# Kernel optimization log

Measured on AMD Instinct MI355X. Metric: run time of the kernel, lower is better.

The kernel has to match this reference:

```python
import jax, jax.numpy as jnp
import numpy as np

B, C, N = 8, 512, 2048
C4 = C // 4


def setup_inputs() -> dict:
    key = jax.random.key(0)
    ks = jax.random.split(key, 10)
    s = lambda fan: 1.0 / np.sqrt(fan)
    return {
        "x": jax.random.normal(ks[0], (B, C, N), jnp.float32),
        "query": jax.random.normal(ks[1], (B, C, N), jnp.float32),
        "mask": jax.random.randint(ks[2], (B, N), 0, 2, jnp.int32),
        "wqk": jax.random.normal(ks[3], (C4, C), jnp.float32) * s(C),  # shared q/k 1x1 conv
        "wv": jax.random.normal(ks[4], (C, C), jnp.float32) * s(C),
        "bv": jax.random.normal(ks[5], (C,), jnp.float32) * 0.01,
        "wt": jax.random.normal(ks[6], (C, C), jnp.float32) * s(C),
        "bt": jax.random.normal(ks[7], (C,), jnp.float32) * 0.01,
        "gamma": jnp.ones((C,), jnp.float32),
        "beta": jnp.zeros((C,), jnp.float32),
        "rmean": jax.random.normal(ks[8], (C,), jnp.float32) * 0.01,
        "rvar": jax.random.uniform(ks[9], (C,), jnp.float32, 0.5, 1.5),
    }


def reference(x, query, mask, wqk, wv, bv, wt, bt, gamma, beta, rmean, rvar):
    # 1x1 convs == per-point linears (q and k share weights)
    x_q = jnp.einsum("dc,bcn->bnd", wqk, query)            # [B,N,C4]
    x_k = jnp.einsum("dc,bcn->bdn", wqk, x)                # [B,C4,N]
    x_v = jnp.einsum("dc,bcn->bdn", wv, x) + bv[None, :, None]  # [B,C,N]

    energy = jnp.einsum("bnd,bdm->bnm", x_q, x_k)          # [B,N,N]
    m = mask.astype(bool)
    m2 = m[:, :, None] & m[:, None, :]                     # [B,N,N]
    energy = jnp.where(m2, energy, jnp.float32(-9e15))
    d = 1e-9 + m2.sum(axis=1, keepdims=True).astype(energy.dtype)  # [B,1,N]
    attention = jax.nn.softmax(energy / d, axis=-1)

    x_r = jnp.einsum("bcn,bnm->bcm", x_v, attention)       # [B,C,N]
    h = x - x_r
    h = jnp.einsum("dc,bcn->bdn", wt, h) + bt[None, :, None]
    # BatchNorm1d (eval) + ReLU
    inv = gamma / jnp.sqrt(rvar + 1e-5)
    h = (h - rmean[None, :, None]) * inv[None, :, None] + beta[None, :, None]
    h = jax.nn.relu(h)
    return x + h
```

## Files before the change

### kernel.cpp

```cpp
#include <hip/hip_runtime.h>
#include <math.h>

typedef __bf16 bf16;
typedef bf16 bf16x8 __attribute__((ext_vector_type(8)));
typedef bf16 bf16x4 __attribute__((ext_vector_type(4)));
typedef float f32x4 __attribute__((ext_vector_type(4)));
typedef unsigned long long u64;

constexpr int kB = 8, kC = 512, kC4 = 128, kN = 2048;

#define MFMA16(a, b, c) __builtin_amdgcn_mfma_f32_16x16x32_bf16(a, b, c, 0, 0, 0)
#define MFMA8(a, b, c) \
  __builtin_amdgcn_mfma_f32_16x16x32_fp8_fp8(a, b, c, 0, 0, 0)

__device__ __forceinline__ unsigned pack4_fp8(float a, float b, float c,
                                              float d) {
  unsigned v = 0;
  v = __builtin_amdgcn_cvt_pk_fp8_f32(a, b, v, false);
  v = __builtin_amdgcn_cvt_pk_fp8_f32(c, d, v, true);
  return v;
}

__global__ __launch_bounds__(256) void k_prep(
    const int* __restrict__ mask, const float* __restrict__ wqk,
    const float* __restrict__ wv, const float* __restrict__ wt,
    const float* __restrict__ gamma, const float* __restrict__ rvar,
    float* __restrict__ cnt, bf16* __restrict__ wqk_bf,
    bf16* __restrict__ wv_bf, bf16* __restrict__ wt_bf,
    float* __restrict__ invg, float* __restrict__ Ssum) {
  const int t = threadIdx.x;
  if (blockIdx.x < 8) {
    const int b = blockIdx.x;
    int s = 0;
    for (int i = t; i < kN; i += 256) s += mask[b * kN + i];
    __shared__ int red[256];
    red[t] = s;
    __syncthreads();
    for (int off = 128; off > 0; off >>= 1) {
      if (t < off) red[t] += red[t + off];
      __syncthreads();
    }
    if (t == 0) cnt[b] = (float)red[0];
    return;
  }
  const int total = 65536 + 262144 + 262144 + 512 + 16384;
  for (int i = (blockIdx.x - 8) * 256 + t; i < total; i += 128 * 256) {
    if (i < 65536) {
      wqk_bf[i] = (bf16)wqk[i];
    } else if (i < 327680) {
      wv_bf[i - 65536] = (bf16)wv[i - 65536];
    } else if (i < 589824) {
      wt_bf[i - 327680] = (bf16)wt[i - 327680];
    } else if (i < 590336) {
      const int j = i - 589824;
      invg[j] = gamma[j] * rsqrtf(rvar[j] + 1e-5f);
    } else {
      Ssum[i - 590336] = 0.0f;
    }
  }
}

__global__ __launch_bounds__(256) void k_tr2(const float* __restrict__ Q,
                                             const float* __restrict__ X,
                                             bf16* __restrict__ XTq,
                                             bf16* __restrict__ XTx) {
  __shared__ float tile[32][69];
  const int z = blockIdx.z, b = z & 7;
  const float* Xs = (z < 8) ? Q : X;
  bf16* XT = (z < 8) ? XTq : XTx;
  const int c0 = blockIdx.y * 32, n0 = blockIdx.x * 64;
  const int t = threadIdx.x;
  const int cc = t >> 4, n4 = (t & 15) * 4;
#pragma unroll
  for (int p = 0; p < 2; p++) {
    const int c = p * 16 + cc;
    const f32x4 v =
        *(const f32x4*)&Xs[((size_t)(b * kC + c0 + c)) * kN + n0 + n4];
    tile[c][n4 + 0] = v[0];
    tile[c][n4 + 1] = v[1];
    tile[c][n4 + 2] = v[2];
    tile[c][n4 + 3] = v[3];
  }
  __syncthreads();
  const int n = t >> 2, c8 = (t & 3) * 8;
  bf16x8 o;
#pragma unroll
  for (int j = 0; j < 8; j++) o[j] = (bf16)tile[c8 + j][n];
  *(bf16x8*)&XT[((size_t)(b * kN + n0 + n)) * kC + c0 + c8] = o;
}

__global__ __launch_bounds__(256, 2) void k_projQK(
    const bf16* __restrict__ XTq, const bf16* __restrict__ XTx,
    const bf16* __restrict__ W, bf16* __restrict__ qT, bf16* __restrict__ kT) {
  __shared__ __align__(16) bf16 As[2][128][32];
  __shared__ __align__(16) bf16 Bs[2][128][32];
  const int nb = blockIdx.x, b = blockIdx.y, src = blockIdx.z;
  const bf16* XT = src ? XTx : XTq;
  bf16* OT = src ? kT : qT;
  const int n0 = nb * 128;
  const int t_ = threadIdx.x, w = t_ >> 6, l = t_ & 63, lo4 = l & 15, g = l >> 4;
  const int mh = w >> 1, ch = w & 1;
  const int srow = w * 16 + (l >> 2), sch = l & 3;
  const int spos = sch ^ ((l >> 3) & 3);
  const int rpos = g ^ ((lo4 >> 1) & 3);
  const bf16* gA0 = &XT[((size_t)(b * kN + n0 + srow)) * kC + sch * 8];
  const bf16* gA1 = gA0 + (size_t)64 * kC;
  const bf16* gB0 = &W[(size_t)srow * kC + sch * 8];
  const bf16* gB1 = gB0 + (size_t)64 * kC;
  f32x4 acc[4][4] = {};
  bf16x8 ra0, ra1, rb0, rb1;
  ra0 = *(const bf16x8*)&gA0[0];
  ra1 = *(const bf16x8*)&gA1[0];
  rb0 = *(const bf16x8*)&gB0[0];
  rb1 = *(const bf16x8*)&gB1[0];
  *(bf16x8*)&As[0][srow][spos * 8] = ra0;
  *(bf16x8*)&As[0][srow + 64][spos * 8] = ra1;
  *(bf16x8*)&Bs[0][srow][spos * 8] = rb0;
  *(bf16x8*)&Bs[0][srow + 64][spos * 8] = rb1;
  __syncthreads();
  for (int tt = 0; tt < 16; tt++) {
    const int buf = tt & 1;
    if (tt < 15) {
      const int k0 = (tt + 1) * 32;
      ra0 = *(const bf16x8*)&gA0[k0];
      ra1 = *(const bf16x8*)&gA1[k0];
      rb0 = *(const bf16x8*)&gB0[k0];
      rb1 = *(const bf16x8*)&gB1[k0];
    }
    bf16x8 af[4], bfr[4];
#pragma unroll
    for (int nf = 0; nf < 4; nf++)
      af[nf] = *(const bf16x8*)&As[buf][mh * 64 + nf * 16 + lo4][rpos * 8];
#pragma unroll
    for (int cf = 0; cf < 4; cf++)
      bfr[cf] = *(const bf16x8*)&Bs[buf][ch * 64 + cf * 16 + lo4][rpos * 8];
#pragma unroll
    for (int nf = 0; nf < 4; nf++)
#pragma unroll
      for (int cf = 0; cf < 4; cf++)
        acc[nf][cf] = MFMA16(af[nf], bfr[cf], acc[nf][cf]);
    if (tt < 15) {
      *(bf16x8*)&As[buf ^ 1][srow][spos * 8] = ra0;
      *(bf16x8*)&As[buf ^ 1][srow + 64][spos * 8] = ra1;
      *(bf16x8*)&Bs[buf ^ 1][srow][spos * 8] = rb0;
      *(bf16x8*)&Bs[buf ^ 1][srow + 64][spos * 8] = rb1;
    }
    __syncthreads();
  }
  bf16* bncw = ((bf16*)As) + w * 16 * 72;
#pragma unroll
  for (int nf = 0; nf < 4; nf++) {
    const int nbase = n0 + mh * 64 + nf * 16;
#pragma unroll
    for (int cf = 0; cf < 4; cf++)
#pragma unroll
      for (int r = 0; r < 4; r++)
        bncw[(4 * g + r) * 72 + cf * 16 + lo4] = (bf16)acc[nf][cf][r];
    const int rr = l >> 2, seg = (l & 3) * 16;
    const bf16x8 v0 = *(const bf16x8*)&bncw[rr * 72 + seg];
    const bf16x8 v1 = *(const bf16x8*)&bncw[rr * 72 + seg + 8];
    bf16* orow = &OT[((size_t)(b * kN + nbase + rr)) * kC4 + ch * 64 + seg];
    *(bf16x8*)&orow[0] = v0;
    *(bf16x8*)&orow[8] = v1;
  }
}

__global__ __launch_bounds__(256, 2) void k_projV(
    const bf16* __restrict__ XTx, const bf16* __restrict__ Wv,
    const float* __restrict__ bv, bf16* __restrict__ xv2) {
  __shared__ __align__(16) bf16 As[2][128][32];
  __shared__ __align__(16) bf16 Bs[2][128][32];
  const int blk = blockIdx.x;
  const int b = blk & 7, tile = blk >> 3;
  const int cb = tile & 3, nb = tile >> 2;
  const int n0 = nb * 128, c0 = cb * 128;
  const int t_ = threadIdx.x, w = t_ >> 6, l = t_ & 63, lo4 = l & 15, g = l >> 4;
  const int mh = w >> 1, ch = w & 1;
  const int srow = w * 16 + (l >> 2), sch = l & 3;
  const int spos = sch ^ ((l >> 3) & 3);
  const int rpos = g ^ ((lo4 >> 1) & 3);
  const bf16* gA0 = &XTx[((size_t)(b * kN + n0 + srow)) * kC + sch * 8];
  const bf16* gA1 = gA0 + (size_t)64 * kC;
  const bf16* gB0 = &Wv[(size_t)(c0 + srow) * kC + sch * 8];
  const bf16* gB1 = gB0 + (size_t)64 * kC;
  f32x4 acc[4][4] = {};
  bf16x8 ra0, ra1, rb0, rb1;
  ra0 = *(const bf16x8*)&gA0[0];
  ra1 = *(const bf16x8*)&gA1[0];
  rb0 = *(const bf16x8*)&gB0[0];
  rb1 = *(const bf16x8*)&gB1[0];
  *(bf16x8*)&As[0][srow][spos * 8] = ra0;
  *(bf16x8*)&As[0][srow + 64][spos * 8] = ra1;
  *(bf16x8*)&Bs[0][srow][spos * 8] = rb0;
  *(bf16x8*)&Bs[0][srow + 64][spos * 8] = rb1;
  __syncthreads();
  for (int tt = 0; tt < 16; tt++) {
    const int buf = tt & 1;
    if (tt < 15) {
      const int k0 = (tt + 1) * 32;
      ra0 = *(const bf16x8*)&gA0[k0];
      ra1 = *(const bf16x8*)&gA1[k0];
      rb0 = *(const bf16x8*)&gB0[k0];
      rb1 = *(const bf16x8*)&gB1[k0];
    }
    bf16x8 af[4], bfr[4];
#pragma unroll
    for (int nf = 0; nf < 4; nf++)
      af[nf] = *(const bf16x8*)&As[buf][mh * 64 + nf * 16 + lo4][rpos * 8];
#pragma unroll
    for (int cf = 0; cf < 4; cf++)
      bfr[cf] = *(const bf16x8*)&Bs[buf][ch * 64 + cf * 16 + lo4][rpos * 8];
#pragma unroll
    for (int nf = 0; nf < 4; nf++)
#pragma unroll
      for (int cf = 0; cf < 4; cf++)
        acc[nf][cf] = MFMA16(af[nf], bfr[cf], acc[nf][cf]);
    if (tt < 15) {
      *(bf16x8*)&As[buf ^ 1][srow][spos * 8] = ra0;
      *(bf16x8*)&As[buf ^ 1][srow + 64][spos * 8] = ra1;
      *(bf16x8*)&Bs[buf ^ 1][srow][spos * 8] = rb0;
      *(bf16x8*)&Bs[buf ^ 1][srow + 64][spos * 8] = rb1;
    }
    __syncthreads();
  }
#pragma unroll
  for (int cf = 0; cf < 4; cf++) {
    const int c = c0 + ch * 64 + cf * 16 + lo4;
    const float bvv = bv[c];
#pragma unroll
    for (int nf = 0; nf < 4; nf++) {
      const int nbase = n0 + mh * 64 + nf * 16 + g * 4;
      bf16x4 o;
#pragma unroll
      for (int r = 0; r < 4; r++) o[r] = (bf16)(acc[nf][cf][r] + bvv);
      *(bf16x4*)&xv2[(((size_t)b * 32 + (nbase >> 6)) * kC + c) * 64 +
                     (nbase & 63)] = o;
    }
  }
}

__global__ __launch_bounds__(256) void k_sum(
    const bf16* __restrict__ qT, const bf16* __restrict__ kT,
    const int* __restrict__ mask, const float* __restrict__ cnt,
    unsigned char* __restrict__ UT8, float* __restrict__ Ssum) {
  __shared__ __align__(16) bf16 kts[2][64][128];
  __shared__ __align__(16) unsigned Ubuf[64][16];
  __shared__ int mss[2][64];
  const int blk = blockIdx.x;
  const int b = blk & 7, nb = (blk >> 3) & 31, mh2 = blk >> 8;
  const int m00 = mh2 * 1024;
  const int t_ = threadIdx.x, w = t_ >> 6, l = t_ & 63, lo4 = l & 15, g = l >> 4;
  const float invd = 1.0f / (cnt[b] + 1e-9f);
  const int n0 = nb * 64;
  bf16x8 aq[4];
#pragma unroll
  for (int ks = 0; ks < 4; ks++)
    aq[ks] = *(const bf16x8*)&qT[((size_t)(b * kN + n0 + w * 16 + lo4)) * kC4 +
                                 ks * 32 + g * 8];
  const int nq = n0 + w * 16 + g * 4;
  const int4 mi = *(const int4*)&mask[b * kN + nq];
  const int mn4[4] = {mi.x, mi.y, mi.z, mi.w};
  float rs4[4] = {0.0f, 0.0f, 0.0f, 0.0f};
  bf16x8 rg[4];
#pragma unroll
  for (int i = 0; i < 4; i++) {
    const int row = w * 16 + i * 4 + g;
    const int q = (l & 15) ^ (row & 7);
    rg[i] = *(const bf16x8*)&kT[((size_t)(b * kN + m00 + row)) * kC4 + q * 8];
  }
#pragma unroll
  for (int i = 0; i < 4; i++) {
    const int row = w * 16 + i * 4 + g;
    *(bf16x8*)&kts[0][row][(l & 15) * 8] = rg[i];
  }
  if (t_ < 16)
    *(int4*)&mss[0][t_ * 4] = *(const int4*)&mask[b * kN + m00 + t_ * 4];
  __syncthreads();
  for (int tt = 0; tt < 16; tt++) {
    const int buf = tt & 1;
    if (tt < 15) {
      const int m0 = m00 + (tt + 1) * 64;
#pragma unroll
      for (int i = 0; i < 4; i++) {
        const int row = w * 16 + i * 4 + g;
        const int q = (l & 15) ^ (row & 7);
        rg[i] = *(const bf16x8*)&kT[((size_t)(b * kN + m0 + row)) * kC4 + q * 8];
      }
    }
#pragma unroll
    for (int mf = 0; mf < 4; mf++) {
      f32x4 e = {};
#pragma unroll
      for (int ks = 0; ks < 4; ks++) {
        const bf16x8 bk =
            *(const bf16x8*)&kts[buf][mf * 16 + lo4]
                                 [((ks * 4 + g) ^ (lo4 & 7)) * 8];
        e = MFMA16(aq[ks], bk, e);
      }
      const int mmv = mss[buf][mf * 16 + lo4];
      float u[4];
#pragma unroll
      for (int r = 0; r < 4; r++) {
        u[r] = mmv ? (mn4[r] ? __expf(e[r] * invd) : 1.0f) : 0.0f;
        rs4[r] += u[r];
      }
      Ubuf[mf * 16 + lo4][(w * 4 + g) ^ lo4] =
          pack4_fp8(u[0], u[1], u[2], u[3]);
    }
    __syncthreads();
    if (tt < 15) {
#pragma unroll
      for (int i = 0; i < 4; i++) {
        const int row = w * 16 + i * 4 + g;
        *(bf16x8*)&kts[buf ^ 1][row][(l & 15) * 8] = rg[i];
      }
      if (t_ < 16)
        *(int4*)&mss[buf ^ 1][t_ * 4] =
            *(const int4*)&mask[b * kN + m00 + (tt + 1) * 64 + t_ * 4];
    }
    {
      const int row = t_ >> 2, q = t_ & 3;
      int4 pkt;
      pkt.x = (int)Ubuf[row][(q * 4 + 0) ^ (row & 15)];
      pkt.y = (int)Ubuf[row][(q * 4 + 1) ^ (row & 15)];
      pkt.z = (int)Ubuf[row][(q * 4 + 2) ^ (row & 15)];
      pkt.w = (int)Ubuf[row][(q * 4 + 3) ^ (row & 15)];
      *(int4*)&UT8[((size_t)(b * kN + m00 + tt * 64 + row)) * kN + n0 +
                   q * 16] = pkt;
    }
    __syncthreads();
  }
#pragma unroll
  for (int r = 0; r < 4; r++) {
#pragma unroll
    for (int off = 1; off < 16; off <<= 1) rs4[r] += __shfl_xor(rs4[r], off);
  }
  if (lo4 == 0) {
#pragma unroll
    for (int r = 0; r < 4; r++) atomicAdd(&Ssum[b * kN + nq + r], rs4[r]);
  }
}

__global__ __launch_bounds__(256) void k_scale(const bf16* __restrict__ xv2,
                                               const float* __restrict__ Ssum,
                                               unsigned* __restrict__ xv8) {
  const int blk = blockIdx.x;
  const int b = blk & 7, part = blk >> 3;
  const size_t base = (size_t)b * (32 * kC * 64);
  for (int it = 0; it < 4; it++) {
    const int chunk = part * 1024 + it * 256 + threadIdx.x;
    const size_t e = (size_t)chunk * 8;
    const int n = ((int)(e >> 15)) * 64 + ((int)e & 63);
    const bf16x8 v = *(const bf16x8*)&xv2[base + e];
    const f32x4 ss0 = *(const f32x4*)&Ssum[b * kN + n];
    const f32x4 ss1 = *(const f32x4*)&Ssum[b * kN + n + 4];
    f32x4 s0, s1;
#pragma unroll
    for (int j = 0; j < 4; j++) {
      s0[j] = 1.0f / ss0[j];
      s1[j] = 1.0f / ss1[j];
    }
    uint2 o;
    o.x = pack4_fp8((float)v[0] * s0[0], (float)v[1] * s0[1],
                    (float)v[2] * s0[2], (float)v[3] * s0[3]);
    o.y = pack4_fp8((float)v[4] * s1[0], (float)v[5] * s1[1],
                    (float)v[6] * s1[2], (float)v[7] * s1[3]);
    *(uint2*)&xv8[(base + e) >> 2] = o;
  }
}

__global__ __launch_bounds__(256, 2) void k_attn2(
    const unsigned char* __restrict__ UT8,
    const unsigned char* __restrict__ xv8, const float* __restrict__ x,
    bf16* __restrict__ hT) {
  __shared__ __align__(16) unsigned char As[2][128][128];
  __shared__ __align__(16) unsigned char Bs[2][128][128];
  const int blk = blockIdx.x;
  const int b = blk & 7, tile = blk >> 3;
  const int cb = tile & 3, mb = tile >> 2;
  const int m0 = mb * 128, c0 = cb * 128;
  const int t_ = threadIdx.x, w = t_ >> 6, l = t_ & 63, lo4 = l & 15, g = l >> 4;
  const int mh = w >> 1, ch = w & 1;
  const int srow = t_ >> 1, psl = t_ & 1;
  const int swk = srow & 15;
  const unsigned char* gA = &UT8[((size_t)(b * kN + m0 + srow)) * kN + psl * 64];
  const unsigned char* gB =
      &xv8[(((size_t)b * 32 + psl) * kC + c0 + srow) * 64];
  f32x4 acc[4][4] = {};
  ulonglong2 eA[4], eB[4], oA[4], oB[4];
#define LOADSET(RA, RB, T)                                                     \
  {                                                                            \
    _Pragma("unroll") for (int q = 0; q < 4; q++) {                            \
      RA[q] = *(const ulonglong2*)&gA[(size_t)(T)*128 + q * 16];               \
      RB[q] = *(const ulonglong2*)&gB[(size_t)(T)*65536 + q * 16];             \
    }                                                                          \
  }
#define STORE_TILE(BUF, RA, RB)                                                \
  {                                                                            \
    _Pragma("unroll") for (int j = 0; j < 8; j++) {                            \
      const int v = (psl * 8 + j) ^ swk;                                       \
      const u64 va = (j & 1) ? RA[j >> 1].y : RA[j >> 1].x;                    \
      const u64 vb = (j & 1) ? RB[j >> 1].y : RB[j >> 1].x;                    \
      *(u64*)&As[BUF][srow][v * 8] = va;                                       \
      *(u64*)&Bs[BUF][srow][v * 8] = vb;                                       \
    }                                                                          \
  }
#define FRAGS_MFMA(BUF)                                                        \
  {                                                                            \
    _Pragma("unroll") for (int ks = 0; ks < 4; ks++) {                         \
      long af[4], bfr[4];                                                      \
      _Pragma("unroll") for (int mf = 0; mf < 4; mf++) af[mf] =                \
          *(const long*)&As[BUF][mh * 64 + mf * 16 + lo4]                      \
                            [((ks * 4 + g) ^ lo4) * 8];                        \
      _Pragma("unroll") for (int cf = 0; cf < 4; cf++) bfr[cf] =               \
          *(const long*)&Bs[BUF][ch * 64 + cf * 16 + lo4]                      \
                            [((ks * 4 + g) ^ lo4) * 8];                        \
      _Pragma("unroll") for (int mf = 0; mf < 4; mf++)                         \
          _Pragma("unroll") for (int cf = 0; cf < 4; cf++) acc[mf][cf] =       \
              MFMA8(af[mf], bfr[cf], acc[mf][cf]);                             \
    }                                                                          \
  }
  LOADSET(eA, eB, 0);
  STORE_TILE(0, eA, eB);
  LOADSET(oA, oB, 1);
  __syncthreads();
  for (int tt2 = 0; tt2 < 16; tt2 += 2) {
    if (tt2 + 2 < 16) LOADSET(eA, eB, tt2 + 2);
    FRAGS_MFMA(0);
    STORE_TILE(1, oA, oB);
    __syncthreads();
    if (tt2 + 3 < 16) LOADSET(oA, oB, tt2 + 3);
    FRAGS_MFMA(1);
    if (tt2 + 2 < 16) STORE_TILE(0, eA, eB);
    __syncthreads();
  }
#undef FRAGS_MFMA
#undef STORE_TILE
#undef LOADSET
  bf16* bncw = ((bf16*)As) + w * 16 * 72;
#pragma unroll
  for (int mf = 0; mf < 4; mf++) {
    const int mbase = m0 + mh * 64 + mf * 16;
    float hh[4][4];
#pragma unroll
    for (int cf = 0; cf < 4; cf++) {
      const int c = c0 + ch * 64 + cf * 16 + lo4;
      const f32x4 xval =
          *(const f32x4*)&x[((size_t)(b * kC + c)) * kN + mbase + g * 4];
#pragma unroll
      for (int r = 0; r < 4; r++) hh[cf][r] = xval[r] - acc[mf][cf][r];
    }
#pragma unroll
    for (int cf = 0; cf < 4; cf++)
#pragma unroll
      for (int r = 0; r < 4; r++)
        bncw[(4 * g + r) * 72 + cf * 16 + lo4] = (bf16)hh[cf][r];
    {
      const int rr = l >> 2, seg = (l & 3) * 16;
      const bf16x8 v0 = *(const bf16x8*)&bncw[rr * 72 + seg];
      const bf16x8 v1 = *(const bf16x8*)&bncw[rr * 72 + seg + 8];
      bf16* orow =
          &hT[((size_t)(b * kN + mbase + rr)) * kC + c0 + ch * 64 + seg];
      *(bf16x8*)&orow[0] = v0;
      *(bf16x8*)&orow[8] = v1;
    }
  }
}

__global__ __launch_bounds__(256, 2) void k_final(
    const bf16* __restrict__ hT, const bf16* __restrict__ wt_bf,
    const float* __restrict__ x, const float* __restrict__ bt,
    const float* __restrict__ beta, const float* __restrict__ rmean,
    const float* __restrict__ invg, float* __restrict__ out) {
  __shared__ __align__(16) bf16 As[2][128][32];
  __shared__ __align__(16) bf16 Bs[2][128][32];
  const int blk = blockIdx.x;
  const int b = blk & 7, tile = blk >> 3;
  const int cb = tile & 3, nb = tile >> 2;
  const int n0 = nb * 128, c0 = cb * 128;
  const int t_ = threadIdx.x, w = t_ >> 6, l = t_ & 63, lo4 = l & 15, g = l >> 4;
  const int mh = w >> 1, ch = w & 1;
  const int srow = w * 16 + (l >> 2), sch = l & 3;
  const int spos = sch ^ ((l >> 3) & 3);
  const int rpos = g ^ ((lo4 >> 1) & 3);
  const bf16* gA0 = &hT[((size_t)(b * kN + n0 + srow)) * kC + sch * 8];
  const bf16* gA1 = gA0 + (size_t)64 * kC;
  const bf16* gB0 = &wt_bf[(size_t)(c0 + srow) * kC + sch * 8];
  const bf16* gB1 = gB0 + (size_t)64 * kC;
  f32x4 acc[4][4] = {};
  bf16x8 ra0, ra1, rb0, rb1;
  ra0 = *(const bf16x8*)&gA0[0];
  ra1 = *(const bf16x8*)&gA1[0];
  rb0 = *(const bf16x8*)&gB0[0];
  rb1 = *(const bf16x8*)&gB1[0];
  *(bf16x8*)&As[0][srow][spos * 8] = ra0;
  *(bf16x8*)&As[0][srow + 64][spos * 8] = ra1;
  *(bf16x8*)&Bs[0][srow][spos * 8] = rb0;
  *(bf16x8*)&Bs[0][srow + 64][spos * 8] = rb1;
  __syncthreads();
  for (int tt = 0; tt < 16; tt++) {
    const int buf = tt & 1;
    if (tt < 15) {
      const int k0 = (tt + 1) * 32;
      ra0 = *(const bf16x8*)&gA0[k0];
      ra1 = *(const bf16x8*)&gA1[k0];
      rb0 = *(const bf16x8*)&gB0[k0];
      rb1 = *(const bf16x8*)&gB1[k0];
    }
    bf16x8 af[4], bfr[4];
#pragma unroll
    for (int nf = 0; nf < 4; nf++)
      af[nf] = *(const bf16x8*)&As[buf][mh * 64 + nf * 16 + lo4][rpos * 8];
#pragma unroll
    for (int cf = 0; cf < 4; cf++)
      bfr[cf] = *(const bf16x8*)&Bs[buf][ch * 64 + cf * 16 + lo4][rpos * 8];
#pragma unroll
    for (int nf = 0; nf < 4; nf++)
#pragma unroll
      for (int cf = 0; cf < 4; cf++)
        acc[nf][cf] = MFMA16(af[nf], bfr[cf], acc[nf][cf]);
    if (tt < 15) {
      *(bf16x8*)&As[buf ^ 1][srow][spos * 8] = ra0;
      *(bf16x8*)&As[buf ^ 1][srow + 64][spos * 8] = ra1;
      *(bf16x8*)&Bs[buf ^ 1][srow][spos * 8] = rb0;
      *(bf16x8*)&Bs[buf ^ 1][srow + 64][spos * 8] = rb1;
    }
    __syncthreads();
  }
#pragma unroll
  for (int cf = 0; cf < 4; cf++) {
    const int c = c0 + ch * 64 + cf * 16 + lo4;
    const float btv = bt[c], rmv = rmean[c], igv = invg[c], bev = beta[c];
#pragma unroll
    for (int nf = 0; nf < 4; nf++) {
      const int nbase = n0 + mh * 64 + nf * 16 + g * 4;
      const size_t base = ((size_t)(b * kC + c)) * kN + nbase;
      const f32x4 xval = *(const f32x4*)&x[base];
      f32x4 o;
#pragma unroll
      for (int r = 0; r < 4; r++) {
        float v = (acc[nf][cf][r] + btv - rmv) * igv + bev;
        v = fmaxf(v, 0.0f);
        o[r] = xval[r] + v;
      }
      *(f32x4*)&out[base] = o;
    }
  }
}

extern "C" void kernel_launch(void* const* d_in, const int* in_sizes, int n_in,
                              void* d_out, int out_size, void* d_ws,
                              size_t ws_size, hipStream_t stream) {
  const float* x = (const float*)d_in[0];
  const float* query = (const float*)d_in[1];
  const int* mask = (const int*)d_in[2];
  const float* wqk = (const float*)d_in[3];
  const float* wv = (const float*)d_in[4];
  const float* bv = (const float*)d_in[5];
  const float* wt = (const float*)d_in[6];
  const float* bt = (const float*)d_in[7];
  const float* gamma = (const float*)d_in[8];
  const float* beta = (const float*)d_in[9];
  const float* rmean = (const float*)d_in[10];
  const float* rvar = (const float*)d_in[11];
  float* out = (float*)d_out;
  char* wsb = (char*)d_ws;

  const size_t MB = 1024 * 1024;
  unsigned char* UT8 = (unsigned char*)wsb;
  bf16* trbufQ = (bf16*)wsb;
  bf16* trbufX = (bf16*)(wsb + 16 * MB);
  bf16* xv2 = (bf16*)(wsb + 32 * MB);
  unsigned* xv8 = (unsigned*)(wsb + 48 * MB);
  bf16* hT = (bf16*)(wsb + 56 * MB);
  bf16* qT = (bf16*)(wsb + 64 * MB);
  bf16* kT = (bf16*)(wsb + 68 * MB);
  bf16* wqk_bf = (bf16*)(wsb + 72 * MB);
  bf16* wv_bf = wqk_bf + 65536;
  bf16* wt_bf = wv_bf + 262144;
  float* invg = (float*)(wt_bf + 262144);
  float* Ssum = invg + 512;
  float* cnt = Ssum + kB * kN;

  k_prep<<<136, 256, 0, stream>>>(mask, wqk, wv, wt, gamma, rvar, cnt, wqk_bf,
                                  wv_bf, wt_bf, invg, Ssum);
  k_tr2<<<dim3(kN / 64, kC / 32, 16), 256, 0, stream>>>(query, x, trbufQ,
                                                        trbufX);
  k_projQK<<<dim3(16, kB, 2), 256, 0, stream>>>(trbufQ, trbufX, wqk_bf, qT,
                                                kT);
  k_projV<<<512, 256, 0, stream>>>(trbufX, wv_bf, bv, xv2);
  k_sum<<<512, 256, 0, stream>>>(qT, kT, mask, cnt, UT8, Ssum);
  k_scale<<<1024, 256, 0, stream>>>(xv2, Ssum, xv8);
  k_attn2<<<512, 256, 0, stream>>>(UT8, (const unsigned char*)xv8, x, hT);
  k_final<<<512, 256, 0, stream>>>(hT, wt_bf, x, bt, beta, rmean, invg, out);
}
```

Measured before the change: 147.3 us.

## Use FP8 Q/K for energy MFMA and fuse row-sum scaling into V projection

Result: faster. 133.9 us (median of 2 runs) (-9.1%).

```diff
diff --git a/kernel.cpp b/kernel.cpp
--- a/kernel.cpp
+++ b/kernel.cpp
@@ -91,12 +91,13 @@
 
 __global__ __launch_bounds__(256, 2) void k_projQK(
     const bf16* __restrict__ XTq, const bf16* __restrict__ XTx,
-    const bf16* __restrict__ W, bf16* __restrict__ qT, bf16* __restrict__ kT) {
+    const bf16* __restrict__ W, unsigned char* __restrict__ qT8,
+    unsigned char* __restrict__ kT8) {
   __shared__ __align__(16) bf16 As[2][128][32];
   __shared__ __align__(16) bf16 Bs[2][128][32];
   const int nb = blockIdx.x, b = blockIdx.y, src = blockIdx.z;
   const bf16* XT = src ? XTx : XTq;
-  bf16* OT = src ? kT : qT;
+  unsigned char* OT8 = src ? kT8 : qT8;
   const int n0 = nb * 128;
   const int t_ = threadIdx.x, w = t_ >> 6, l = t_ & 63, lo4 = l & 15, g = l >> 4;
   const int mh = w >> 1, ch = w & 1;
@@ -159,15 +160,118 @@
     const int rr = l >> 2, seg = (l & 3) * 16;
     const bf16x8 v0 = *(const bf16x8*)&bncw[rr * 72 + seg];
     const bf16x8 v1 = *(const bf16x8*)&bncw[rr * 72 + seg + 8];
-    bf16* orow = &OT[((size_t)(b * kN + nbase + rr)) * kC4 + ch * 64 + seg];
-    *(bf16x8*)&orow[0] = v0;
-    *(bf16x8*)&orow[8] = v1;
+    int4 o;
+    o.x = (int)pack4_fp8((float)v0[0], (float)v0[1], (float)v0[2],
+                         (float)v0[3]);
+    o.y = (int)pack4_fp8((float)v0[4], (float)v0[5], (float)v0[6],
+                         (float)v0[7]);
+    o.z = (int)pack4_fp8((float)v1[0], (float)v1[1], (float)v1[2],
+                         (float)v1[3]);
+    o.w = (int)pack4_fp8((float)v1[4], (float)v1[5], (float)v1[6],
+                         (float)v1[7]);
+    *(int4*)&OT8[((size_t)(b * kN + nbase + rr)) * kC4 + ch * 64 + seg] = o;
+  }
+}
+
+__global__ __launch_bounds__(256) void k_sum(
+    const unsigned char* __restrict__ qT8, const unsigned char* __restrict__ kT8,
+    const int* __restrict__ mask, const float* __restrict__ cnt,
+    unsigned char* __restrict__ UT8, float* __restrict__ Ssum) {
+  __shared__ __align__(16) unsigned char kts[2][64][128];
+  __shared__ __align__(16) unsigned Ubuf[64][16];
+  __shared__ int mss[2][64];
+  const int blk = blockIdx.x;
+  const int b = blk & 7, nb = (blk >> 3) & 31, mh2 = blk >> 8;
+  const int m00 = mh2 * 1024;
+  const int t_ = threadIdx.x, w = t_ >> 6, l = t_ & 63, lo4 = l & 15, g = l >> 4;
+  const float invd = 1.0f / (cnt[b] + 1e-9f);
+  const int n0 = nb * 64;
+  u64 aq[4];
+#pragma unroll
+  for (int ks = 0; ks < 4; ks++)
+    aq[ks] = *(const u64*)&qT8[((size_t)(b * kN + n0 + w * 16 + lo4)) * kC4 +
+                               ks * 32 + g * 8];
+  const int nq = n0 + w * 16 + g * 4;
+  const int4 mi = *(const int4*)&mask[b * kN + nq];
+  const int mn4[4] = {mi.x, mi.y, mi.z, mi.w};
+  float rs4[4] = {0.0f, 0.0f, 0.0f, 0.0f};
+  const int srow = t_ >> 2, sq = t_ & 3;
+  const int swk = srow & 15;
+  u64 rg[4];
+#pragma unroll
+  for (int j = 0; j < 4; j++)
+    rg[j] = *(const u64*)&kT8[((size_t)(b * kN + m00 + srow)) * kC4 + sq * 32 +
+                              j * 8];
+#pragma unroll
+  for (int j = 0; j < 4; j++)
+    *(u64*)&kts[0][srow][((sq * 4 + j) ^ swk) * 8] = rg[j];
+  if (t_ < 16)
+    *(int4*)&mss[0][t_ * 4] = *(const int4*)&mask[b * kN + m00 + t_ * 4];
+  __syncthreads();
+  for (int tt = 0; tt < 16; tt++) {
+    const int buf = tt & 1;
+    if (tt < 15) {
+      const int m0 = m00 + (tt + 1) * 64;
+#pragma unroll
+      for (int j = 0; j < 4; j++)
+        rg[j] = *(const u64*)&kT8[((size_t)(b * kN + m0 + srow)) * kC4 +
+                                  sq * 32 + j * 8];
+    }
+#pragma unroll
+    for (int mf = 0; mf < 4; mf++) {
+      f32x4 e = {};
+#pragma unroll
+      for (int ks = 0; ks < 4; ks++) {
+        const long bk =
+            *(const long*)&kts[buf][mf * 16 + lo4][((ks * 4 + g) ^ lo4) * 8];
+        e = MFMA8((long)aq[ks], bk, e);
+      }
+      const int mmv = mss[buf][mf * 16 + lo4];
+      float u[4];
+#pragma unroll
+      for (int r = 0; r < 4; r++) {
+        u[r] = mmv ? (mn4[r] ? __expf(e[r] * invd) : 1.0f) : 0.0f;
+        rs4[r] += u[r];
+      }
+      Ubuf[mf * 16 + lo4][(w * 4 + g) ^ lo4] =
+          pack4_fp8(u[0], u[1], u[2], u[3]);
+    }
+    __syncthreads();
+    if (tt < 15) {
+#pragma unroll
+      for (int j = 0; j < 4; j++)
+        *(u64*)&kts[buf ^ 1][srow][((sq * 4 + j) ^ swk) * 8] = rg[j];
+      if (t_ < 16)
+        *(int4*)&mss[buf ^ 1][t_ * 4] =
+            *(const int4*)&mask[b * kN + m00 + (tt + 1) * 64 + t_ * 4];
+    }
+    {
+      const int row = t_ >> 2, q = t_ & 3;
+      int4 pkt;
+      pkt.x = (int)Ubuf[row][(q * 4 + 0) ^ (row & 15)];
+      pkt.y = (int)Ubuf[row][(q * 4 + 1) ^ (row & 15)];
+      pkt.z = (int)Ubuf[row][(q * 4 + 2) ^ (row & 15)];
+      pkt.w = (int)Ubuf[row][(q * 4 + 3) ^ (row & 15)];
+      *(int4*)&UT8[((size_t)(b * kN + m00 + tt * 64 + row)) * kN + n0 +
+                   q * 16] = pkt;
+    }
+    __syncthreads();
+  }
+#pragma unroll
+  for (int r = 0; r < 4; r++) {
+#pragma unroll
+    for (int off = 1; off < 16; off <<= 1) rs4[r] += __shfl_xor(rs4[r], off);
+  }
+  if (lo4 == 0) {
+#pragma unroll
+    for (int r = 0; r < 4; r++) atomicAdd(&Ssum[b * kN + nq + r], rs4[r]);
   }
 }
 
 __global__ __launch_bounds__(256, 2) void k_projV(
     const bf16* __restrict__ XTx, const bf16* __restrict__ Wv,
-    const float* __restrict__ bv, bf16* __restrict__ xv2) {
+    const float* __restrict__ bv, const float* __restrict__ Ssum,
+    unsigned char* __restrict__ xv8) {
   __shared__ __align__(16) bf16 As[2][128][32];
   __shared__ __align__(16) bf16 Bs[2][128][32];
   const int blk = blockIdx.x;
@@ -224,148 +328,23 @@
     __syncthreads();
   }
 #pragma unroll
-  for (int cf = 0; cf < 4; cf++) {
-    const int c = c0 + ch * 64 + cf * 16 + lo4;
-    const float bvv = bv[c];
-#pragma unroll
-    for (int nf = 0; nf < 4; nf++) {
-      const int nbase = n0 + mh * 64 + nf * 16 + g * 4;
-      bf16x4 o;
-#pragma unroll
-      for (int r = 0; r < 4; r++) o[r] = (bf16)(acc[nf][cf][r] + bvv);
-      *(bf16x4*)&xv2[(((size_t)b * 32 + (nbase >> 6)) * kC + c) * 64 +
-                     (nbase & 63)] = o;
-    }
-  }
-}
-
-__global__ __launch_bounds__(256) void k_sum(
-    const bf16* __restrict__ qT, const bf16* __restrict__ kT,
-    const int* __restrict__ mask, const float* __restrict__ cnt,
-    unsigned char* __restrict__ UT8, float* __restrict__ Ssum) {
-  __shared__ __align__(16) bf16 kts[2][64][128];
-  __shared__ __align__(16) unsigned Ubuf[64][16];
-  __shared__ int mss[2][64];
-  const int blk = blockIdx.x;
-  const int b = blk & 7, nb = (blk >> 3) & 31, mh2 = blk >> 8;
-  const int m00 = mh2 * 1024;
-  const int t_ = threadIdx.x, w = t_ >> 6, l = t_ & 63, lo4 = l & 15, g = l >> 4;
-  const float invd = 1.0f / (cnt[b] + 1e-9f);
-  const int n0 = nb * 64;
-  bf16x8 aq[4];
-#pragma unroll
-  for (int ks = 0; ks < 4; ks++)
-    aq[ks] = *(const bf16x8*)&qT[((size_t)(b * kN + n0 + w * 16 + lo4)) * kC4 +
-                                 ks * 32 + g * 8];
-  const int nq = n0 + w * 16 + g * 4;
-  const int4 mi = *(const int4*)&mask[b * kN + nq];
-  const int mn4[4] = {mi.x, mi.y, mi.z, mi.w};
-  float rs4[4] = {0.0f, 0.0f, 0.0f, 0.0f};
-  bf16x8 rg[4];
-#pragma unroll
-  for (int i = 0; i < 4; i++) {
-    const int row = w * 16 + i * 4 + g;
-    const int q = (l & 15) ^ (row & 7);
-    rg[i] = *(const bf16x8*)&kT[((size_t)(b * kN + m00 + row)) * kC4 + q * 8];
-  }
-#pragma unroll
-  for (int i = 0; i < 4; i++) {
-    const int row = w * 16 + i * 4 + g;
-    *(bf16x8*)&kts[0][row][(l & 15) * 8] = rg[i];
-  }
-  if (t_ < 16)
-    *(int4*)&mss[0][t_ * 4] = *(const int4*)&mask[b * kN + m00 + t_ * 4];
-  __syncthreads();
-  for (int tt = 0; tt < 16; tt++) {
-    const int buf = tt & 1;
-    if (tt < 15) {
-      const int m0 = m00 + (tt + 1) * 64;
-#pragma unroll
-      for (int i = 0; i < 4; i++) {
-        const int row = w * 16 + i * 4 + g;
-        const int q = (l & 15) ^ (row & 7);
-        rg[i] = *(const bf16x8*)&kT[((size_t)(b * kN + m0 + row)) * kC4 + q * 8];
-      }
-    }
-#pragma unroll
-    for (int mf = 0; mf < 4; mf++) {
-      f32x4 e = {};
-#pragma unroll
-      for (int ks = 0; ks < 4; ks++) {
-        const bf16x8 bk =
-            *(const bf16x8*)&kts[buf][mf * 16 + lo4]
-                                 [((ks * 4 + g) ^ (lo4 & 7)) * 8];
-        e = MFMA16(aq[ks], bk, e);
-      }
-      const int mmv = mss[buf][mf * 16 + lo4];
-      float u[4];
-#pragma unroll
-      for (int r = 0; r < 4; r++) {
-        u[r] = mmv ? (mn4[r] ? __expf(e[r] * invd) : 1.0f) : 0.0f;
-        rs4[r] += u[r];
-      }
-      Ubuf[mf * 16 + lo4][(w * 4 + g) ^ lo4] =
-          pack4_fp8(u[0], u[1], u[2], u[3]);
-    }
-    __syncthreads();
-    if (tt < 15) {
-#pragma unroll
-      for (int i = 0; i < 4; i++) {
-        const int row = w * 16 + i * 4 + g;
-        *(bf16x8*)&kts[buf ^ 1][row][(l & 15) * 8] = rg[i];
-      }
-      if (t_ < 16)
-        *(int4*)&mss[buf ^ 1][t_ * 4] =
-            *(const int4*)&mask[b * kN + m00 + (tt + 1) * 64 + t_ * 4];
-    }
-    {
-      const int row = t_ >> 2, q = t_ & 3;
-      int4 pkt;
-      pkt.x = (int)Ubuf[row][(q * 4 + 0) ^ (row & 15)];
-      pkt.y = (int)Ubuf[row][(q * 4 + 1) ^ (row & 15)];
-      pkt.z = (int)Ubuf[row][(q * 4 + 2) ^ (row & 15)];
-      pkt.w = (int)Ubuf[row][(q * 4 + 3) ^ (row & 15)];
-      *(int4*)&UT8[((size_t)(b * kN + m00 + tt * 64 + row)) * kN + n0 +
-                   q * 16] = pkt;
-    }
-    __syncthreads();
-  }
-#pragma unroll
-  for (int r = 0; r < 4; r++) {
-#pragma unroll
-    for (int off = 1; off < 16; off <<= 1) rs4[r] += __shfl_xor(rs4[r], off);
-  }
-  if (lo4 == 0) {
-#pragma unroll
-    for (int r = 0; r < 4; r++) atomicAdd(&Ssum[b * kN + nq + r], rs4[r]);
-  }
-}
-
-__global__ __launch_bounds__(256) void k_scale(const bf16* __restrict__ xv2,
-                                               const float* __restrict__ Ssum,
-                                               unsigned* __restrict__ xv8) {
-  const int blk = blockIdx.x;
-  const int b = blk & 7, part = blk >> 3;
-  const size_t base = (size_t)b * (32 * kC * 64);
-  for (int it = 0; it < 4; it++) {
-    const int chunk = part * 1024 + it * 256 + threadIdx.x;
-    const size_t e = (size_t)chunk * 8;
-    const int n = ((int)(e >> 15)) * 64 + ((int)e & 63);
-    const bf16x8 v = *(const bf16x8*)&xv2[base + e];
-    const f32x4 ss0 = *(const f32x4*)&Ssum[b * kN + n];
-    const f32x4 ss1 = *(const f32x4*)&Ssum[b * kN + n + 4];
-    f32x4 s0, s1;
-#pragma unroll
-    for (int j = 0; j < 4; j++) {
-      s0[j] = 1.0f / ss0[j];
-      s1[j] = 1.0f / ss1[j];
-    }
-    uint2 o;
-    o.x = pack4_fp8((float)v[0] * s0[0], (float)v[1] * s0[1],
-                    (float)v[2] * s0[2], (float)v[3] * s0[3]);
-    o.y = pack4_fp8((float)v[4] * s1[0], (float)v[5] * s1[1],
-                    (float)v[6] * s1[2], (float)v[7] * s1[3]);
-    *(uint2*)&xv8[(base + e) >> 2] = o;
+  for (int nf = 0; nf < 4; nf++) {
+    const int nbase = n0 + mh * 64 + nf * 16 + g * 4;
+    const f32x4 ssv = *(const f32x4*)&Ssum[b * kN + nbase];
+    f32x4 s;
+#pragma unroll
+    for (int r = 0; r < 4; r++) s[r] = 256.0f / ssv[r];
+#pragma unroll
+    for (int cf = 0; cf < 4; cf++) {
+      const int c = c0 + ch * 64 + cf * 16 + lo4;
+      const float bvv = bv[c];
+      const unsigned o = pack4_fp8((acc[nf][cf][0] + bvv) * s[0],
+                                   (acc[nf][cf][1] + bvv) * s[1],
+                                   (acc[nf][cf][2] + bvv) * s[2],
+                                   (acc[nf][cf][3] + bvv) * s[3]);
+      *(unsigned*)&xv8[(((size_t)b * 32 + (nbase >> 6)) * kC + c) * 64 +
+                       (nbase & 63)] = o;
+    }
   }
 }
 
@@ -448,7 +427,8 @@
       const f32x4 xval =
           *(const f32x4*)&x[((size_t)(b * kC + c)) * kN + mbase + g * 4];
 #pragma unroll
-      for (int r = 0; r < 4; r++) hh[cf][r] = xval[r] - acc[mf][cf][r];
+      for (int r = 0; r < 4; r++)
+        hh[cf][r] = xval[r] - acc[mf][cf][r] * 0.00390625f;
     }
 #pragma unroll
     for (int cf = 0; cf < 4; cf++)
@@ -568,14 +548,13 @@
 
   const size_t MB = 1024 * 1024;
   unsigned char* UT8 = (unsigned char*)wsb;
-  bf16* trbufQ = (bf16*)wsb;
-  bf16* trbufX = (bf16*)(wsb + 16 * MB);
-  bf16* xv2 = (bf16*)(wsb + 32 * MB);
-  unsigned* xv8 = (unsigned*)(wsb + 48 * MB);
-  bf16* hT = (bf16*)(wsb + 56 * MB);
-  bf16* qT = (bf16*)(wsb + 64 * MB);
-  bf16* kT = (bf16*)(wsb + 68 * MB);
-  bf16* wqk_bf = (bf16*)(wsb + 72 * MB);
+  unsigned char* xv8 = (unsigned char*)(wsb + 32 * MB);
+  bf16* hT = (bf16*)(wsb + 40 * MB);
+  unsigned char* qT8 = (unsigned char*)(wsb + 48 * MB);
+  unsigned char* kT8 = (unsigned char*)(wsb + 50 * MB);
+  bf16* trbufQ = (bf16*)(wsb + 52 * MB);
+  bf16* trbufX = (bf16*)(wsb + 68 * MB);
+  bf16* wqk_bf = (bf16*)(wsb + 84 * MB);
   bf16* wv_bf = wqk_bf + 65536;
   bf16* wt_bf = wv_bf + 262144;
   float* invg = (float*)(wt_bf + 262144);
@@ -586,11 +565,10 @@
                                   wv_bf, wt_bf, invg, Ssum);
   k_tr2<<<dim3(kN / 64, kC / 32, 16), 256, 0, stream>>>(query, x, trbufQ,
                                                         trbufX);
-  k_projQK<<<dim3(16, kB, 2), 256, 0, stream>>>(trbufQ, trbufX, wqk_bf, qT,
-                                                kT);
-  k_projV<<<512, 256, 0, stream>>>(trbufX, wv_bf, bv, xv2);
-  k_sum<<<512, 256, 0, stream>>>(qT, kT, mask, cnt, UT8, Ssum);
-  k_scale<<<1024, 256, 0, stream>>>(xv2, Ssum, xv8);
-  k_attn2<<<512, 256, 0, stream>>>(UT8, (const unsigned char*)xv8, x, hT);
+  k_projQK<<<dim3(16, kB, 2), 256, 0, stream>>>(trbufQ, trbufX, wqk_bf, qT8,
+                                                kT8);
+  k_sum<<<512, 256, 0, stream>>>(qT8, kT8, mask, cnt, UT8, Ssum);
+  k_projV<<<512, 256, 0, stream>>>(trbufX, wv_bf, bv, Ssum, xv8);
+  k_attn2<<<512, 256, 0, stream>>>(UT8, xv8, x, hT);
   k_final<<<512, 256, 0, stream>>>(hT, wt_bf, x, bt, beta, rmean, invg, out);
 }
```
